# Kernel optimization log

Measured on AMD Instinct MI355X. Metric: run time of the kernel, lower is better.

Reference implementation:

```python
import jax, jax.numpy as jnp
import numpy as np

SCALE = 30.0
MARGIN = 0.5
COS_M = float(np.cos(MARGIN))
SIN_M = float(np.sin(MARGIN))
TH = float(np.cos(np.pi - MARGIN))
MM = float(np.sin(np.pi - MARGIN) * MARGIN)
LN_EPS = 1e-7

B, S, H = 16, 2048, 1024
N_SPANS = 64
N_CLASSES = 4096


def setup_inputs() -> dict:
    key = jax.random.key(0)
    k1, k2, k3, k4, k5 = jax.random.split(key, 5)
    encoder_layer = jax.random.normal(k1, (B, S, H), dtype=jnp.float32)
    ln_gamma = jnp.ones((H,), jnp.float32)
    ln_beta = jnp.zeros((H,), jnp.float32)
    # xavier-uniform-like init for arcface head weight [out, in]
    limit = float(np.sqrt(6.0 / (N_CLASSES + H)))
    arc_weight = jax.random.uniform(k2, (N_CLASSES, H), jnp.float32, -limit, limit)
    heads = jax.random.randint(k3, (B, N_SPANS), 0, S - 32).astype(jnp.int32)
    lens = jax.random.randint(k4, (B, N_SPANS), 1, 33).astype(jnp.int32)
    tails = heads + lens  # guaranteed head < tail <= S
    labels = jax.random.randint(k5, (B, N_SPANS), 0, N_CLASSES).astype(jnp.int32)
    return {
        "encoder_layer": encoder_layer,
        "ln_gamma": ln_gamma,
        "ln_beta": ln_beta,
        "arc_weight": arc_weight,
        "span_head_idxs": heads,
        "span_tail_idxs": tails,
        "labels": labels,
    }


def _span_mean(encoder_layer, heads, tails):
    # fused ragged segment-mean via inclusive prefix sums over the seq dim
    # csum: [B, S+1, H], csum[b, t] = sum of encoder_layer[b, :t]
    csum = jnp.concatenate(
        [jnp.zeros_like(encoder_layer[:, :1]), jnp.cumsum(encoder_layer, axis=1)], axis=1
    )
    gather = lambda idx: jnp.take_along_axis(csum, idx[:, :, None].astype(jnp.int32), axis=1)
    sums = gather(tails) - gather(heads)  # [B, n_spans, H]
    counts = (tails - heads).astype(encoder_layer.dtype)[:, :, None]
    return sums / counts


def _layer_norm(x, gamma, beta):
    mu = jnp.mean(x, axis=-1, keepdims=True)
    var = jnp.mean(jnp.square(x - mu), axis=-1, keepdims=True)
    return (x - mu) * jax.lax.rsqrt(var + LN_EPS) * gamma + beta


def _l2norm(x):
    return x / jnp.maximum(jnp.linalg.norm(x, axis=-1, keepdims=True), 1e-12)


def reference(encoder_layer, ln_gamma, ln_beta, arc_weight, span_head_idxs, span_tail_idxs, labels):
    emb = _span_mean(encoder_layer, span_head_idxs, span_tail_idxs)  # [B, n_spans, H]
    emb = _layer_norm(emb, ln_gamma, ln_beta)
    emb = emb.reshape(-1, emb.shape[-1])  # [B*n_spans, H]
    lab = labels.reshape(-1)
    # ArcMarginProduct: cosine similarity
    cosine = (_l2norm(emb) @ _l2norm(arc_weight).T).astype(jnp.float32)  # [N, C]
    sine = jnp.sqrt(jnp.clip(1.0 - jnp.square(cosine), 0.0))
    phi = cosine * COS_M - sine * SIN_M
    phi = jnp.where(cosine > TH, phi, cosine - MM)
    onehot = jax.nn.one_hot(lab, cosine.shape[-1], dtype=cosine.dtype)
    logits = (onehot * phi + (1.0 - onehot) * cosine) * SCALE
    # mean cross entropy (all labels valid, ignore_index unused)
    logp = jax.nn.log_softmax(logits, axis=-1)
    nll = -jnp.take_along_axis(logp, lab[:, None].astype(jnp.int32), axis=1)[:, 0]
    return jnp.mean(nll)
```

## Files before the change

### kernel.cpp

```cpp
#include <hip/hip_runtime.h>
#include <math.h>

#define B_     16
#define S_     2048
#define H_     1024
#define NS_    64
#define NC_    4096
#define NROWS  1024

#define SCALE_ 30.0f
#define COS_M_ 0.8775825618903728f
#define SIN_M_ 0.479425538604203f
#define TH_    (-0.8775825618903728f)
#define MM_    0.2397127693021015f
#define LN_EPS_ 1e-7f


__device__ __forceinline__ unsigned short f2bf(float f) {
    union { float f; unsigned int u; } v; v.f = f;
    unsigned int r = v.u + 0x7fffu + ((v.u >> 16) & 1u);
    return (unsigned short)(r >> 16);
}

__device__ __forceinline__ float block_sum(float v) {
    __shared__ float sb[4];
    #pragma unroll
    for (int off = 32; off > 0; off >>= 1) v += __shfl_down(v, off, 64);
    if ((threadIdx.x & 63) == 0) sb[threadIdx.x >> 6] = v;
    __syncthreads();
    float r = sb[0] + sb[1] + sb[2] + sb[3];
    __syncthreads();
    return r;
}

__device__ __forceinline__ float block_max(float v) {
    __shared__ float sb[4];
    #pragma unroll
    for (int off = 32; off > 0; off >>= 1) v = fmaxf(v, __shfl_down(v, off, 64));
    if ((threadIdx.x & 63) == 0) sb[threadIdx.x >> 6] = v;
    __syncthreads();
    float r = fmaxf(fmaxf(sb[0], sb[1]), fmaxf(sb[2], sb[3]));
    __syncthreads();
    return r;
}

__device__ __forceinline__ void gload16(const void* g, void* l) {
    __builtin_amdgcn_global_load_lds(
        (const __attribute__((address_space(1))) unsigned int*)g,
        (__attribute__((address_space(3))) unsigned int*)l,
        16, 0, 0);
}

typedef short bf16x8 __attribute__((ext_vector_type(8)));
typedef float f32x4  __attribute__((ext_vector_type(4)));

__global__ __launch_bounds__(256) void fused_norm_kernel(
    const float* __restrict__ enc,
    const float* __restrict__ gamma,
    const float* __restrict__ beta,
    const int*   __restrict__ heads,
    const int*   __restrict__ tails,
    const float* __restrict__ W,
    unsigned short* __restrict__ embn,
    unsigned short* __restrict__ Wn,
    unsigned int*   __restrict__ cnt)
{
    const int tid = threadIdx.x;
    if (blockIdx.x == 0 && tid == 0) *cnt = 0u;

    if (blockIdx.x < NROWS) {
        const int span = blockIdx.x;
        const int b    = span >> 6;
        const int head = heads[span];
        const int tail = tails[span];
        const int cnt_ = tail - head;

        const float4* base = (const float4*)(enc + ((size_t)b * S_ + head) * H_) + tid;
        float4 a0 = {0.f,0.f,0.f,0.f}, a1 = a0, a2 = a0, a3 = a0;
        int s = 0;
        for (; s + 4 <= cnt_; s += 4) {
            float4 x0 = base[(size_t)(s + 0) * (H_ / 4)];
            float4 x1 = base[(size_t)(s + 1) * (H_ / 4)];
            float4 x2 = base[(size_t)(s + 2) * (H_ / 4)];
            float4 x3 = base[(size_t)(s + 3) * (H_ / 4)];
            a0.x += x0.x; a0.y += x0.y; a0.z += x0.z; a0.w += x0.w;
            a1.x += x1.x; a1.y += x1.y; a1.z += x1.z; a1.w += x1.w;
            a2.x += x2.x; a2.y += x2.y; a2.z += x2.z; a2.w += x2.w;
            a3.x += x3.x; a3.y += x3.y; a3.z += x3.z; a3.w += x3.w;
        }
        for (; s < cnt_; ++s) {
            float4 x = base[(size_t)s * (H_ / 4)];
            a0.x += x.x; a0.y += x.y; a0.z += x.z; a0.w += x.w;
        }
        const float inv = 1.0f / (float)cnt_;
        float v0 = (a0.x + a1.x + a2.x + a3.x) * inv;
        float v1 = (a0.y + a1.y + a2.y + a3.y) * inv;
        float v2 = (a0.z + a1.z + a2.z + a3.z) * inv;
        float v3 = (a0.w + a1.w + a2.w + a3.w) * inv;

        float mu = block_sum(v0 + v1 + v2 + v3) * (1.0f / H_);
        float d0 = v0 - mu, d1 = v1 - mu, d2 = v2 - mu, d3 = v3 - mu;
        float var = block_sum(d0*d0 + d1*d1 + d2*d2 + d3*d3) * (1.0f / H_);
        float rstd = rsqrtf(var + LN_EPS_);

        const float4 g4 = ((const float4*)gamma)[tid];
        const float4 b4 = ((const float4*)beta)[tid];
        float y0 = d0 * rstd * g4.x + b4.x;
        float y1 = d1 * rstd * g4.y + b4.y;
        float y2 = d2 * rstd * g4.z + b4.z;
        float y3 = d3 * rstd * g4.w + b4.w;

        float ss = block_sum(y0*y0 + y1*y1 + y2*y2 + y3*y3);
        float invn = 1.0f / fmaxf(sqrtf(ss), 1e-12f);

        ushort4 o;
        o.x = f2bf(y0 * invn); o.y = f2bf(y1 * invn);
        o.z = f2bf(y2 * invn); o.w = f2bf(y3 * invn);
        *(ushort4*)(embn + (size_t)span * H_ + tid * 4) = o;
    } else {
        const int row = blockIdx.x - NROWS;
        float4 x = ((const float4*)(W + (size_t)row * H_))[tid];
        float ss = block_sum(x.x*x.x + x.y*x.y + x.z*x.z + x.w*x.w);
        float invn = 1.0f / fmaxf(sqrtf(ss), 1e-12f);
        ushort4 o;
        o.x = f2bf(x.x * invn); o.y = f2bf(x.y * invn);
        o.z = f2bf(x.z * invn); o.w = f2bf(x.w * invn);
        *(ushort4*)(Wn + (size_t)row * H_ + tid * 4) = o;
    }
}

__global__ __launch_bounds__(256, 2) void gemm_kernel(
    const unsigned short* __restrict__ A,
    const unsigned short* __restrict__ Bw,
    float* __restrict__ C)
{
    __shared__ short As[2][128 * 64];
    __shared__ short Bs[2][128 * 64];

    const int bid = blockIdx.y * 8 + blockIdx.x;
    const int swz = (bid & 7) * 32 + (bid >> 3);
    const int m0  = (swz & 7) * 128;
    const int n0  = (swz >> 3) * 128;

    const int tid  = threadIdx.x;
    const int lane = tid & 63;
    const int w    = tid >> 6;
    const int wm   = (w & 1) * 64;
    const int wn   = (w >> 1) * 64;
    const int lrow = lane & 15;
    const int q    = lane >> 4;
    const int xr   = lrow & 7;

    f32x4 acc[4][4];
    #pragma unroll
    for (int i = 0; i < 4; ++i)
        #pragma unroll
        for (int j = 0; j < 4; ++j)
            acc[i][j] = (f32x4){0.f, 0.f, 0.f, 0.f};

    auto stage = [&](int bsel, int k0) {
        #pragma unroll
        for (int h = 0; h < 4; ++h) {
            const int s   = tid + h * 256;
            const int row = s >> 3;
            const int s16 = (s & 7) ^ (row & 7);
            gload16(A  + (size_t)(m0 + row) * 1024 + k0 + s16 * 8, &As[bsel][s * 8]);
            gload16(Bw + (size_t)(n0 + row) * 1024 + k0 + s16 * 8, &Bs[bsel][s * 8]);
        }
    };

    auto compute = [&](int bsel) {
        #pragma unroll
        for (int kk = 0; kk < 2; ++kk) {
            const int c16 = ((kk << 2) | q) ^ xr;
            bf16x8 af[4], bfr[4];
            #pragma unroll
            for (int i = 0; i < 4; ++i)
                af[i] = *(const bf16x8*)(&As[bsel][(wm + i * 16 + lrow) * 64 + c16 * 8]);
            #pragma unroll
            for (int j = 0; j < 4; ++j)
                bfr[j] = *(const bf16x8*)(&Bs[bsel][(wn + j * 16 + lrow) * 64 + c16 * 8]);
            #pragma unroll
            for (int i = 0; i < 4; ++i)
                #pragma unroll
                for (int j = 0; j < 4; ++j)
                    acc[i][j] = __builtin_amdgcn_mfma_f32_16x16x32_bf16(af[i], bfr[j], acc[i][j], 0, 0, 0);
        }
    };

    stage(0, 0);
    asm volatile("s_waitcnt vmcnt(0)" ::: "memory");
    __builtin_amdgcn_s_barrier();

    int cur = 0;
    for (int t = 0; t < 15; ++t) {
        stage(cur ^ 1, (t + 1) * 64);
        compute(cur);
        asm volatile("s_waitcnt vmcnt(0)" ::: "memory");
        __builtin_amdgcn_s_barrier();
        cur ^= 1;
    }
    compute(cur);

    #pragma unroll
    for (int i = 0; i < 4; ++i) {
        const int rbase = m0 + wm + i * 16 + q * 4;
        #pragma unroll
        for (int j = 0; j < 4; ++j) {
            const int col = n0 + wn + j * 16 + lrow;
            #pragma unroll
            for (int r2 = 0; r2 < 4; ++r2)
                C[(size_t)(rbase + r2) * NC_ + col] = acc[i][j][r2];
        }
    }
}

__global__ __launch_bounds__(256) void ce_kernel(
    const float* __restrict__ cosine,
    const int*   __restrict__ labels,
    float* __restrict__ nll,
    float* __restrict__ out,
    unsigned int* __restrict__ cnt)
{
    __shared__ float s_lab;
    __shared__ int   s_last;
    const int row = blockIdx.x;
    const int lab = labels[row];
    const int tid = threadIdx.x;
    const float4* c4 = (const float4*)(cosine + (size_t)row * NC_);

    float vals[16];
    float m = -1e30f;
    #pragma unroll
    for (int t = 0; t < 4; ++t) {
        float4 x = c4[tid + t * 256];
        const int cbase = (tid + t * 256) * 4;
        float xs[4] = {x.x, x.y, x.z, x.w};
        #pragma unroll
        for (int k = 0; k < 4; ++k) {
            float c = xs[k];
            float logit = c;
            if (cbase + k == lab) {
                float sine = sqrtf(fmaxf(1.0f - c * c, 0.0f));
                float phi  = c * COS_M_ - sine * SIN_M_;
                logit = (c > TH_) ? phi : (c - MM_);
            }
            logit *= SCALE_;
            vals[t * 4 + k] = logit;
            if (cbase + k == lab) s_lab = logit;
            m = fmaxf(m, logit);
        }
    }
    float gm = block_max(m);
    float e = 0.f;
    #pragma unroll
    for (int t = 0; t < 16; ++t) e += expf(vals[t] - gm);
    float se = block_sum(e);

    if (tid == 0) {
        nll[row] = logf(se) + gm - s_lab;
        __threadfence();
        s_last = (atomicAdd(cnt, 1u) == NROWS - 1);
    }
    __syncthreads();
    if (s_last) {
        __threadfence();
        float s = 0.f;
        #pragma unroll
        for (int t = 0; t < 4; ++t) s += nll[tid + t * 256];
        float tot = block_sum(s);
        if (tid == 0) out[0] = tot * (1.0f / NROWS);
    }
}

extern "C" void kernel_launch(void* const* d_in, const int* in_sizes, int n_in,
                              void* d_out, int out_size, void* d_ws, size_t ws_size,
                              hipStream_t stream) {
    const float* enc    = (const float*)d_in[0];
    const float* gamma  = (const float*)d_in[1];
    const float* beta   = (const float*)d_in[2];
    const float* W      = (const float*)d_in[3];
    const int*   heads  = (const int*)d_in[4];
    const int*   tails  = (const int*)d_in[5];
    const int*   labels = (const int*)d_in[6];
    float* out = (float*)d_out;

    char* ws = (char*)d_ws;
    unsigned short* embn   = (unsigned short*)(ws);
    unsigned short* Wn     = (unsigned short*)(ws + (2u  << 20));
    float*          cosine = (float*)        (ws + (10u << 20));
    float*          nllbuf = (float*)        (ws + (26u << 20));
    unsigned int*   cnt    = (unsigned int*) (ws + (26u << 20) + 8192);

    fused_norm_kernel<<<NROWS + NC_, 256, 0, stream>>>(enc, gamma, beta, heads, tails, W, embn, Wn, cnt);
    dim3 g3(8, 32);
    gemm_kernel <<<g3,  256, 0, stream>>>(embn, Wn, cosine);
    ce_kernel   <<<NROWS, 256, 0, stream>>>(cosine, labels, nllbuf, out, cnt);
}
```

Baseline: 239.7 us.

## Fuse ArcFace margin and per-tile softmax stats into GEMM epilogue, triple-buffer

The GEMM epilogue now applies the ArcFace margin, computes per-row max and sum-of-exp for each 128-column tile, and writes only these partial statistics instead of the full 1024x4096 cosine matrix. A small combine kernel merges the 32 tile partials per row with the log-sum-exp rescaling and computes the mean NLL. The GEMM main loop also moves from double to triple buffering with partial vmcnt waits. This removes a 16 MB write and re-read, at the cost of more LDS and one block per CU.

```diff
diff --git a/kernel.cpp b/kernel.cpp
--- a/kernel.cpp
+++ b/kernel.cpp
@@ -7,6 +7,7 @@
 #define NS_    64
 #define NC_    4096
 #define NROWS  1024
+#define NTILES 32
 
 #define SCALE_ 30.0f
 #define COS_M_ 0.8775825618903728f
@@ -29,17 +30,6 @@
     if ((threadIdx.x & 63) == 0) sb[threadIdx.x >> 6] = v;
     __syncthreads();
     float r = sb[0] + sb[1] + sb[2] + sb[3];
-    __syncthreads();
-    return r;
-}
-
-__device__ __forceinline__ float block_max(float v) {
-    __shared__ float sb[4];
-    #pragma unroll
-    for (int off = 32; off > 0; off >>= 1) v = fmaxf(v, __shfl_down(v, off, 64));
-    if ((threadIdx.x & 63) == 0) sb[threadIdx.x >> 6] = v;
-    __syncthreads();
-    float r = fmaxf(fmaxf(sb[0], sb[1]), fmaxf(sb[2], sb[3]));
     __syncthreads();
     return r;
 }
@@ -129,24 +119,31 @@
     }
 }
 
-__global__ __launch_bounds__(256, 2) void gemm_kernel(
+__global__ __launch_bounds__(256, 1) void gemm_ce_kernel(
     const unsigned short* __restrict__ A,
     const unsigned short* __restrict__ Bw,
-    float* __restrict__ C)
+    const int*   __restrict__ labels,
+    float* __restrict__ tmax,
+    float* __restrict__ tsum,
+    float* __restrict__ glab)
 {
-    __shared__ short As[2][128 * 64];
-    __shared__ short Bs[2][128 * 64];
+    __shared__ short As[3][128 * 64];
+    __shared__ short Bs[3][128 * 64];
+    __shared__ float smx[2][128];
+    __shared__ float ssm[2][128];
 
     const int bid = blockIdx.y * 8 + blockIdx.x;
     const int swz = (bid & 7) * 32 + (bid >> 3);
     const int m0  = (swz & 7) * 128;
-    const int n0  = (swz >> 3) * 128;
+    const int nt  = swz >> 3;
+    const int n0  = nt * 128;
 
     const int tid  = threadIdx.x;
     const int lane = tid & 63;
     const int w    = tid >> 6;
     const int wm   = (w & 1) * 64;
-    const int wn   = (w >> 1) * 64;
+    const int wnh  = w >> 1;
+    const int wn   = wnh * 64;
     const int lrow = lane & 15;
     const int q    = lane >> 4;
     const int xr   = lrow & 7;
@@ -189,78 +186,153 @@
     };
 
     stage(0, 0);
+    stage(1, 64);
+    asm volatile("s_waitcnt vmcnt(8)" ::: "memory");
+    __builtin_amdgcn_s_barrier();
+    __builtin_amdgcn_sched_barrier(0);
+
+    int cur = 0, nxt = 1, fut = 2;
+    for (int t = 0; t < 14; ++t) {
+        stage(fut, (t + 2) * 64);
+        compute(cur);
+        asm volatile("s_waitcnt vmcnt(8)" ::: "memory");
+        __builtin_amdgcn_s_barrier();
+        __builtin_amdgcn_sched_barrier(0);
+        const int tmp = cur; cur = nxt; nxt = fut; fut = tmp;
+    }
+    compute(cur);
     asm volatile("s_waitcnt vmcnt(0)" ::: "memory");
     __builtin_amdgcn_s_barrier();
-
-    int cur = 0;
-    for (int t = 0; t < 15; ++t) {
-        stage(cur ^ 1, (t + 1) * 64);
-        compute(cur);
-        asm volatile("s_waitcnt vmcnt(0)" ::: "memory");
-        __builtin_amdgcn_s_barrier();
-        cur ^= 1;
-    }
-    compute(cur);
-
-    #pragma unroll
-    for (int i = 0; i < 4; ++i) {
-        const int rbase = m0 + wm + i * 16 + q * 4;
-        #pragma unroll
-        for (int j = 0; j < 4; ++j) {
-            const int col = n0 + wn + j * 16 + lrow;
+    __builtin_amdgcn_sched_barrier(0);
+    compute(nxt);
+
+
+    int lab[4][4];
+    #pragma unroll
+    for (int i = 0; i < 4; ++i)
+        #pragma unroll
+        for (int r2 = 0; r2 < 4; ++r2)
+            lab[i][r2] = labels[m0 + wm + i * 16 + q * 4 + r2];
+
+    #pragma unroll
+    for (int i = 0; i < 4; ++i)
+        #pragma unroll
+        for (int r2 = 0; r2 < 4; ++r2) {
+            const int gcol_base = n0 + wn;
+            #pragma unroll
+            for (int j = 0; j < 4; ++j) {
+                const int col = gcol_base + j * 16 + lrow;
+                float c = acc[i][j][r2];
+                float logit;
+                if (col == lab[i][r2]) {
+                    float sine = sqrtf(fmaxf(1.0f - c * c, 0.0f));
+                    float phi  = c * COS_M_ - sine * SIN_M_;
+                    logit = ((c > TH_) ? phi : (c - MM_)) * SCALE_;
+                    glab[m0 + wm + i * 16 + q * 4 + r2] = logit;
+                } else {
+                    logit = c * SCALE_;
+                }
+                acc[i][j][r2] = logit;
+            }
+        }
+
+    float mrow[4][4];
+    #pragma unroll
+    for (int i = 0; i < 4; ++i)
+        #pragma unroll
+        for (int r2 = 0; r2 < 4; ++r2) {
+            float m = fmaxf(fmaxf(acc[i][0][r2], acc[i][1][r2]),
+                            fmaxf(acc[i][2][r2], acc[i][3][r2]));
+            #pragma unroll
+            for (int mk = 1; mk <= 8; mk <<= 1)
+                m = fmaxf(m, __shfl_xor(m, mk, 64));
+            mrow[i][r2] = m;
+        }
+
+    if (lrow == 0) {
+        #pragma unroll
+        for (int i = 0; i < 4; ++i)
             #pragma unroll
             for (int r2 = 0; r2 < 4; ++r2)
-                C[(size_t)(rbase + r2) * NC_ + col] = acc[i][j][r2];
-        }
-    }
-}
-
-__global__ __launch_bounds__(256) void ce_kernel(
-    const float* __restrict__ cosine,
-    const int*   __restrict__ labels,
+                smx[wnh][wm + i * 16 + q * 4 + r2] = mrow[i][r2];
+    }
+    __syncthreads();
+    float M[4][4];
+    #pragma unroll
+    for (int i = 0; i < 4; ++i)
+        #pragma unroll
+        for (int r2 = 0; r2 < 4; ++r2)
+            M[i][r2] = fmaxf(mrow[i][r2], smx[wnh ^ 1][wm + i * 16 + q * 4 + r2]);
+
+    float srow[4][4];
+    #pragma unroll
+    for (int i = 0; i < 4; ++i)
+        #pragma unroll
+        for (int r2 = 0; r2 < 4; ++r2) {
+            float s = expf(acc[i][0][r2] - M[i][r2]) + expf(acc[i][1][r2] - M[i][r2])
+                    + expf(acc[i][2][r2] - M[i][r2]) + expf(acc[i][3][r2] - M[i][r2]);
+            #pragma unroll
+            for (int mk = 1; mk <= 8; mk <<= 1)
+                s += __shfl_xor(s, mk, 64);
+            srow[i][r2] = s;
+        }
+    if (lrow == 0) {
+        #pragma unroll
+        for (int i = 0; i < 4; ++i)
+            #pragma unroll
+            for (int r2 = 0; r2 < 4; ++r2)
+                ssm[wnh][wm + i * 16 + q * 4 + r2] = srow[i][r2];
+    }
+    __syncthreads();
+    if (wnh == 0 && lrow == 0) {
+        #pragma unroll
+        for (int i = 0; i < 4; ++i)
+            #pragma unroll
+            for (int r2 = 0; r2 < 4; ++r2) {
+                const int rl = wm + i * 16 + q * 4 + r2;
+                const int R  = m0 + rl;
+                tmax[(size_t)R * NTILES + nt] = M[i][r2];
+                tsum[(size_t)R * NTILES + nt] = srow[i][r2] + ssm[1][rl];
+            }
+    }
+}
+
+__global__ __launch_bounds__(256) void combine_kernel(
+    const float* __restrict__ tmax,
+    const float* __restrict__ tsum,
+    const float* __restrict__ glab,
     float* __restrict__ nll,
     float* __restrict__ out,
     unsigned int* __restrict__ cnt)
 {
-    __shared__ float s_lab;
-    __shared__ int   s_last;
-    const int row = blockIdx.x;
-    const int lab = labels[row];
+    __shared__ int s_last;
     const int tid = threadIdx.x;
-    const float4* c4 = (const float4*)(cosine + (size_t)row * NC_);
-
-    float vals[16];
-    float m = -1e30f;
-    #pragma unroll
-    for (int t = 0; t < 4; ++t) {
-        float4 x = c4[tid + t * 256];
-        const int cbase = (tid + t * 256) * 4;
-        float xs[4] = {x.x, x.y, x.z, x.w};
-        #pragma unroll
-        for (int k = 0; k < 4; ++k) {
-            float c = xs[k];
-            float logit = c;
-            if (cbase + k == lab) {
-                float sine = sqrtf(fmaxf(1.0f - c * c, 0.0f));
-                float phi  = c * COS_M_ - sine * SIN_M_;
-                logit = (c > TH_) ? phi : (c - MM_);
-            }
-            logit *= SCALE_;
-            vals[t * 4 + k] = logit;
-            if (cbase + k == lab) s_lab = logit;
-            m = fmaxf(m, logit);
-        }
-    }
-    float gm = block_max(m);
-    float e = 0.f;
-    #pragma unroll
-    for (int t = 0; t < 16; ++t) e += expf(vals[t] - gm);
-    float se = block_sum(e);
+    const int row = blockIdx.x * 256 + tid;
+
+    const float4* mx4 = (const float4*)(tmax + (size_t)row * NTILES);
+    const float4* sm4 = (const float4*)(tsum + (size_t)row * NTILES);
+    float4 mv[8], sv[8];
+    #pragma unroll
+    for (int k = 0; k < 8; ++k) { mv[k] = mx4[k]; sv[k] = sm4[k]; }
+
+    float gm = -1e30f;
+    #pragma unroll
+    for (int k = 0; k < 8; ++k)
+        gm = fmaxf(gm, fmaxf(fmaxf(mv[k].x, mv[k].y), fmaxf(mv[k].z, mv[k].w)));
+
+    float se = 0.f;
+    #pragma unroll
+    for (int k = 0; k < 8; ++k) {
+        se += sv[k].x * expf(mv[k].x - gm);
+        se += sv[k].y * expf(mv[k].y - gm);
+        se += sv[k].z * expf(mv[k].z - gm);
+        se += sv[k].w * expf(mv[k].w - gm);
+    }
+    nll[row] = logf(se) + gm - glab[row];
 
     if (tid == 0) {
-        nll[row] = logf(se) + gm - s_lab;
         __threadfence();
-        s_last = (atomicAdd(cnt, 1u) == NROWS - 1);
+        s_last = (atomicAdd(cnt, 1u) == (NROWS / 256) - 1);
     }
     __syncthreads();
     if (s_last) {
@@ -286,14 +358,16 @@
     float* out = (float*)d_out;
 
     char* ws = (char*)d_ws;
-    unsigned short* embn   = (unsigned short*)(ws);
-    unsigned short* Wn     = (unsigned short*)(ws + (2u  << 20));
-    float*          cosine = (float*)        (ws + (10u << 20));
-    float*          nllbuf = (float*)        (ws + (26u << 20));
-    unsigned int*   cnt    = (unsigned int*) (ws + (26u << 20) + 8192);
+    unsigned short* embn = (unsigned short*)(ws);
+    unsigned short* Wn   = (unsigned short*)(ws + (2u  << 20));
+    float* tmax          = (float*)        (ws + (10u << 20));
+    float* tsum          = (float*)        (ws + (10u << 20) + (128u<<10));
+    float* glab          = (float*)        (ws + (10u << 20) + (256u<<10));
+    float* nllbuf        = (float*)        (ws + (10u << 20) + (260u<<10));
+    unsigned int* cnt    = (unsigned int*) (ws + (10u << 20) + (264u<<10));
 
     fused_norm_kernel<<<NROWS + NC_, 256, 0, stream>>>(enc, gamma, beta, heads, tails, W, embn, Wn, cnt);
     dim3 g3(8, 32);
-    gemm_kernel <<<g3,  256, 0, stream>>>(embn, Wn, cosine);
-    ce_kernel   <<<NROWS, 256, 0, stream>>>(cosine, labels, nllbuf, out, cnt);
-}
+    gemm_ce_kernel <<<g3, 256, 0, stream>>>(embn, Wn, labels, tmax, tsum, glab);
+    combine_kernel <<<NROWS / 256, 256, 0, stream>>>(tmax, tsum, glab, nllbuf, out, cnt);
+}
```

Measured after the change: 228.7 us, median of 2. -4.6%, faster.
